# Optimization experiments

Hardware: AMD Instinct MI355X
Metric: run time of the kernel (lower is better)

The kernel has to match this reference:

```python
import jax, jax.numpy as jnp
import numpy as np

LN_EPS = 1e-3   # keras LayerNormalization default epsilon
EPS = 1e-5      # module's self.eps
QB = 128.0      # 2**(bits-1) with bits=8


def ste_round(x):
    # straight-through round: forward = round(x), backward = identity
    return x + jax.lax.stop_gradient(jnp.round(x) - x)


def setup_inputs() -> dict:
    key = jax.random.key(0)
    k1, k2 = jax.random.split(key)
    x = jax.random.normal(k1, (4, 8192, 1024), dtype=jnp.float32)
    weight = jax.random.normal(k2, (1024, 1024), dtype=jnp.float32) * 0.02
    ln_gamma = jnp.ones((1024,), dtype=jnp.float32)
    ln_beta = jnp.zeros((1024,), dtype=jnp.float32)
    return {"x": x, "weight": weight, "ln_gamma": ln_gamma, "ln_beta": ln_beta}


def reference(x, weight, ln_gamma, ln_beta):
    # LayerNorm over last axis (keras defaults: eps=1e-3, learnable scale/center)
    mu = jnp.mean(x, axis=-1, keepdims=True)
    var = jnp.var(x, axis=-1, keepdims=True)
    xn = (x - mu) * jax.lax.rsqrt(var + LN_EPS) * ln_gamma + ln_beta

    # 1.58-bit weight ternarization with STE round
    beta = jnp.mean(jnp.abs(weight))                     # per-tensor scale
    w_q = jnp.clip(ste_round(weight / (beta + EPS)), -1.0, 1.0)

    # activation quantization (flg_before_linear=True branch)
    gamma = jnp.max(jnp.abs(xn))                         # per-tensor absmax
    xq = jnp.clip(xn * QB / gamma, -QB + EPS, QB - EPS)

    # quantized matmul + fused rescale
    y = jnp.einsum('bsd,du->bsu', xq, w_q)
    return y * (gamma * beta / QB)
```

## Files before the change

kernel.cpp:

```cpp
#include <hip/hip_runtime.h>
#include <stdint.h>


#define M_ROWS 32768
#define KDIM 1024
#define NDIM 1024

typedef int v4i  __attribute__((ext_vector_type(4)));
typedef int v16i __attribute__((ext_vector_type(16)));

__global__ __launch_bounds__(256) void absum_k(const float* __restrict__ w,
                                               float* __restrict__ partials) {
    int idx = blockIdx.x * 256 + threadIdx.x;
    float4 v = ((const float4*)w)[idx];
    float s = fabsf(v.x) + fabsf(v.y) + fabsf(v.z) + fabsf(v.w);
    #pragma unroll
    for (int o = 32; o; o >>= 1) s += __shfl_xor(s, o);
    __shared__ float p[4];
    if ((threadIdx.x & 63) == 0) p[threadIdx.x >> 6] = s;
    __syncthreads();
    if (threadIdx.x == 0) partials[blockIdx.x] = p[0] + p[1] + p[2] + p[3];
}

__global__ __launch_bounds__(256) void quant_k(const float* __restrict__ w,
                                               const float* __restrict__ partials,
                                               char* __restrict__ wqT,
                                               float* __restrict__ wsum) {
    int t = threadIdx.x;
    float s = partials[t] + partials[t + 256] + partials[t + 512] + partials[t + 768];
    #pragma unroll
    for (int o = 32; o; o >>= 1) s += __shfl_xor(s, o);
    __shared__ float ps[4];
    if ((t & 63) == 0) ps[t >> 6] = s;
    __syncthreads();
    float total = ps[0] + ps[1] + ps[2] + ps[3];
    if (blockIdx.x == 0 && t == 0) wsum[0] = total;
    float beta = total * (1.0f / 1048576.0f);
    float inv  = 1.0f / (beta + 1e-5f);

    __shared__ char sT[64 * 80];
    int k0 = (blockIdx.x >> 4) * 64, n0 = (blockIdx.x & 15) * 64;
    int n_l = t & 63;
    #pragma unroll
    for (int r = 0; r < 16; ++r) {
        int k_l = (t >> 6) * 16 + r;
        float q = rintf(w[(size_t)(k0 + k_l) * NDIM + n0 + n_l] * inv);
        q = fminf(1.0f, fmaxf(-1.0f, q));
        sT[n_l * 80 + k_l] = (char)(int)q;
    }
    __syncthreads();
    int nn = t >> 2, c = t & 3;
    v4i val = *(const v4i*)&sT[nn * 80 + c * 16];
    *(v4i*)&wqT[(size_t)(n0 + nn) * KDIM + k0 + c * 16] = val;
}

__global__ __launch_bounds__(256) void ln_gemm_k(const float* __restrict__ x,
                                                 const float* __restrict__ g,
                                                 const float* __restrict__ bln,
                                                 const char* __restrict__ wq,
                                                 const float* __restrict__ wsum,
                                                 float* __restrict__ out) {
    __shared__ char  sA[64 * 1024];
    __shared__ char  sB[64 * 128];
    __shared__ float sScl[64];

    int t = threadIdx.x;
    int w = t >> 6, lane = t & 63;
    int half = lane >> 5, l31 = lane & 31;
    int bm0 = blockIdx.x * 64;

    int bn_l  = t >> 1;
    int bhalf = t & 1;
    int br    = t >> 2;

    v4i buf[2];
    {
        const char* src = wq + ((size_t)bn_l << 10) + bhalf * 32;
        buf[0] = *(const v4i*)(src);
        buf[1] = *(const v4i*)(src + 16);
    }

    float4 g4[4], b4[4];
    #pragma unroll
    for (int j = 0; j < 4; ++j) {
        g4[j] = ((const float4*)g)[lane + 64 * j];
        b4[j] = ((const float4*)bln)[lane + 64 * j];
    }
    #pragma unroll 1
    for (int rr = 0; rr < 16; ++rr) {
        int row = w * 16 + rr;
        const float4* xr = (const float4*)(x + ((size_t)(bm0 + row) << 10));
        float4 v0 = xr[lane], v1 = xr[lane + 64], v2 = xr[lane + 128], v3 = xr[lane + 192];
        float s  = v0.x + v0.y + v0.z + v0.w + v1.x + v1.y + v1.z + v1.w
                 + v2.x + v2.y + v2.z + v2.w + v3.x + v3.y + v3.z + v3.w;
        float ss = v0.x*v0.x + v0.y*v0.y + v0.z*v0.z + v0.w*v0.w
                 + v1.x*v1.x + v1.y*v1.y + v1.z*v1.z + v1.w*v1.w
                 + v2.x*v2.x + v2.y*v2.y + v2.z*v2.z + v2.w*v2.w
                 + v3.x*v3.x + v3.y*v3.y + v3.z*v3.z + v3.w*v3.w;
        #pragma unroll
        for (int o = 32; o; o >>= 1) { s += __shfl_xor(s, o); ss += __shfl_xor(ss, o); }
        float mu  = s * (1.0f / 1024.0f);
        float var = ss * (1.0f / 1024.0f) - mu * mu;
        float rs  = rsqrtf(var + 1e-3f);
        float xn[16];
        float4 vv[4] = {v0, v1, v2, v3};
        float mx = 0.f;
        #pragma unroll
        for (int j = 0; j < 4; ++j) {
            xn[4*j+0] = (vv[j].x - mu) * rs * g4[j].x + b4[j].x;
            xn[4*j+1] = (vv[j].y - mu) * rs * g4[j].y + b4[j].y;
            xn[4*j+2] = (vv[j].z - mu) * rs * g4[j].z + b4[j].z;
            xn[4*j+3] = (vv[j].w - mu) * rs * g4[j].w + b4[j].w;
            #pragma unroll
            for (int e = 0; e < 4; ++e) mx = fmaxf(mx, fabsf(xn[4*j+e]));
        }
        #pragma unroll
        for (int o = 32; o; o >>= 1) mx = fmaxf(mx, __shfl_xor(mx, o));
        mx = fmaxf(mx, 1e-20f);
        float inv = 127.0f / mx;
        if (lane == 0) sScl[row] = mx * (1.0f / 127.0f);
        #pragma unroll
        for (int j = 0; j < 4; ++j) {
            char4 c4;
            c4.x = (char)(int)rintf(xn[4*j+0] * inv);
            c4.y = (char)(int)rintf(xn[4*j+1] * inv);
            c4.z = (char)(int)rintf(xn[4*j+2] * inv);
            c4.w = (char)(int)rintf(xn[4*j+3] * inv);
            int c    = (lane >> 2) + 16 * j;
            int slot = c ^ (row & 7);
            *(char4*)&sA[row * 1024 + slot * 16 + (lane & 3) * 4] = c4;
        }
    }

    {
        #pragma unroll
        for (int q = 0; q < 2; ++q) {
            int slot = (((bn_l & 1) * 4 + bhalf * 2 + q) ^ (br & 7));
            *(v4i*)&sB[br * 128 + slot * 16] = buf[q];
        }
        const char* src = wq + ((size_t)bn_l << 10) + 64 + bhalf * 32;
        buf[0] = *(const v4i*)(src);
        buf[1] = *(const v4i*)(src + 16);
    }
    __syncthreads();

    int wm = w & 1, wn = w >> 1;
    int mrow  = wm * 32 + l31;
    int aBase = mrow * 1024;
    int am7   = mrow & 7;
    int nl0 = wn * 64 + l31;
    int br0 = nl0 >> 1, br1 = (nl0 + 32) >> 1;
    int bs0 = (nl0 & 1) * 4;
    float beta = wsum[0] * (1.0f / 1048576.0f);

    v16i acc[2];
    #pragma unroll
    for (int r = 0; r < 16; ++r) { acc[0][r] = 0; acc[1][r] = 0; }

    for (int it = 0; it < 128; ++it) {
        int kt = it & 15;
        #pragma unroll
        for (int kk = 0; kk < 2; ++kk) {
            int cA = kt * 4 + kk * 2 + half;
            v4i a  = *(const v4i*)&sA[aBase + ((cA ^ am7) << 4)];
            int ct = kk * 2 + half;
            v4i b0 = *(const v4i*)&sB[br0 * 128 + (((bs0 + ct) ^ (br0 & 7)) << 4)];
            v4i b1 = *(const v4i*)&sB[br1 * 128 + (((bs0 + ct) ^ (br1 & 7)) << 4)];
            acc[0] = __builtin_amdgcn_mfma_i32_32x32x32_i8(a, b0, acc[0], 0, 0, 0);
            acc[1] = __builtin_amdgcn_mfma_i32_32x32x32_i8(a, b1, acc[1], 0, 0, 0);
        }
        __syncthreads();
        if (it < 127) {
            #pragma unroll
            for (int q = 0; q < 2; ++q) {
                int slot = (((bn_l & 1) * 4 + bhalf * 2 + q) ^ (br & 7));
                *(v4i*)&sB[br * 128 + slot * 16] = buf[q];
            }
        }
        if (it < 126) {
            int tl = it + 2;
            const char* src = wq + ((size_t)(((tl >> 4) << 7) + bn_l) << 10)
                                 + (tl & 15) * 64 + bhalf * 32;
            buf[0] = *(const v4i*)(src);
            buf[1] = *(const v4i*)(src + 16);
        }
        if (kt == 15) {
            int n0 = it >> 4;
            int colBase = n0 * 128 + wn * 64 + l31;
            #pragma unroll
            for (int r = 0; r < 16; ++r) {
                int rloc = wm * 32 + (r & 3) + 8 * (r >> 2) + 4 * half;
                float sc = sScl[rloc] * beta;
                size_t o = (size_t)(bm0 + rloc) * NDIM + colBase;
                out[o]      = (float)acc[0][r] * sc;
                out[o + 32] = (float)acc[1][r] * sc;
            }
            #pragma unroll
            for (int r = 0; r < 16; ++r) { acc[0][r] = 0; acc[1][r] = 0; }
        }
        __syncthreads();
    }
}

extern "C" void kernel_launch(void* const* d_in, const int* in_sizes, int n_in,
                              void* d_out, int out_size, void* d_ws, size_t ws_size,
                              hipStream_t stream) {
    const float* x        = (const float*)d_in[0];
    const float* weight   = (const float*)d_in[1];
    const float* ln_gamma = (const float*)d_in[2];
    const float* ln_beta  = (const float*)d_in[3];
    float* out = (float*)d_out;

    float* wsum     = (float*)d_ws;
    float* partials = (float*)((char*)d_ws + 4096);
    char*  wqT      = (char*)d_ws + (1u << 18);

    absum_k<<<1024, 256, 0, stream>>>(weight, partials);
    quant_k<<<256, 256, 0, stream>>>(weight, partials, wqT, wsum);
    ln_gemm_k<<<M_ROWS / 64, 256, 0, stream>>>(x, ln_gamma, ln_beta, wqT, wsum, out);
}
```

Baseline: 289.0 us.

## Pre-pack weights into MFMA fragment layout and read B directly from global

The weight quantizer now writes int8 weights in a layout that matches the MFMA B-operand fragments, so the GEMM loads B straight from global/L2 into registers. This removes the shared-memory B staging and the two barriers per k-step. The A tile in LDS is re-laid out per lane, and each wave now computes a 64x128 output tile with 8 accumulators. LayerNorm loads become contiguous per lane. The cost is more register pressure (launch bounds 2) and every block rereading the full weight matrix from global memory.

Result: no change. 283.9 us (-1.8%).

```diff
diff --git a/kernel.cpp b/kernel.cpp
--- a/kernel.cpp
+++ b/kernel.cpp
@@ -24,7 +24,7 @@
 
 __global__ __launch_bounds__(256) void quant_k(const float* __restrict__ w,
                                                const float* __restrict__ partials,
-                                               char* __restrict__ wqT,
+                                               char* __restrict__ wqP,
                                                float* __restrict__ wsum) {
     int t = threadIdx.x;
     float s = partials[t] + partials[t + 256] + partials[t + 512] + partials[t + 768];
@@ -51,17 +51,18 @@
     __syncthreads();
     int nn = t >> 2, c = t & 3;
     v4i val = *(const v4i*)&sT[nn * 80 + c * 16];
-    *(v4i*)&wqT[(size_t)(n0 + nn) * KDIM + k0 + c * 16] = val;
-}
-
-__global__ __launch_bounds__(256) void ln_gemm_k(const float* __restrict__ x,
-                                                 const float* __restrict__ g,
-                                                 const float* __restrict__ bln,
-                                                 const char* __restrict__ wq,
-                                                 const float* __restrict__ wsum,
-                                                 float* __restrict__ out) {
+    int n = n0 + nn, k = k0 + c * 16;
+    int idx = ((n >> 5) * 32 + (k >> 5)) * 64 + (n & 31) + ((k >> 4) & 1) * 32;
+    *(v4i*)&wqP[(size_t)idx * 16] = val;
+}
+
+__global__ __launch_bounds__(256, 2) void ln_gemm_k(const float* __restrict__ x,
+                                                    const float* __restrict__ g,
+                                                    const float* __restrict__ bln,
+                                                    const char* __restrict__ wqP,
+                                                    const float* __restrict__ wsum,
+                                                    float* __restrict__ out) {
     __shared__ char  sA[64 * 1024];
-    __shared__ char  sB[64 * 128];
     __shared__ float sScl[64];
 
     int t = threadIdx.x;
@@ -69,28 +70,17 @@
     int half = lane >> 5, l31 = lane & 31;
     int bm0 = blockIdx.x * 64;
 
-    int bn_l  = t >> 1;
-    int bhalf = t & 1;
-    int br    = t >> 2;
-
-    v4i buf[2];
-    {
-        const char* src = wq + ((size_t)bn_l << 10) + bhalf * 32;
-        buf[0] = *(const v4i*)(src);
-        buf[1] = *(const v4i*)(src + 16);
-    }
-
     float4 g4[4], b4[4];
     #pragma unroll
     for (int j = 0; j < 4; ++j) {
-        g4[j] = ((const float4*)g)[lane + 64 * j];
-        b4[j] = ((const float4*)bln)[lane + 64 * j];
+        g4[j] = ((const float4*)g)[lane * 4 + j];
+        b4[j] = ((const float4*)bln)[lane * 4 + j];
     }
     #pragma unroll 1
     for (int rr = 0; rr < 16; ++rr) {
         int row = w * 16 + rr;
         const float4* xr = (const float4*)(x + ((size_t)(bm0 + row) << 10));
-        float4 v0 = xr[lane], v1 = xr[lane + 64], v2 = xr[lane + 128], v3 = xr[lane + 192];
+        float4 v0 = xr[lane * 4], v1 = xr[lane * 4 + 1], v2 = xr[lane * 4 + 2], v3 = xr[lane * 4 + 3];
         float s  = v0.x + v0.y + v0.z + v0.w + v1.x + v1.y + v1.z + v1.w
                  + v2.x + v2.y + v2.z + v2.w + v3.x + v3.y + v3.z + v3.w;
         float ss = v0.x*v0.x + v0.y*v0.y + v0.z*v0.z + v0.w*v0.w
@@ -119,86 +109,75 @@
         mx = fmaxf(mx, 1e-20f);
         float inv = 127.0f / mx;
         if (lane == 0) sScl[row] = mx * (1.0f / 127.0f);
+        int qw[4];
         #pragma unroll
         for (int j = 0; j < 4; ++j) {
-            char4 c4;
-            c4.x = (char)(int)rintf(xn[4*j+0] * inv);
-            c4.y = (char)(int)rintf(xn[4*j+1] * inv);
-            c4.z = (char)(int)rintf(xn[4*j+2] * inv);
-            c4.w = (char)(int)rintf(xn[4*j+3] * inv);
-            int c    = (lane >> 2) + 16 * j;
-            int slot = c ^ (row & 7);
-            *(char4*)&sA[row * 1024 + slot * 16 + (lane & 3) * 4] = c4;
-        }
-    }
-
-    {
-        #pragma unroll
-        for (int q = 0; q < 2; ++q) {
-            int slot = (((bn_l & 1) * 4 + bhalf * 2 + q) ^ (br & 7));
-            *(v4i*)&sB[br * 128 + slot * 16] = buf[q];
-        }
-        const char* src = wq + ((size_t)bn_l << 10) + 64 + bhalf * 32;
-        buf[0] = *(const v4i*)(src);
-        buf[1] = *(const v4i*)(src + 16);
-    }
-    __syncthreads();
-
-    int wm = w & 1, wn = w >> 1;
-    int mrow  = wm * 32 + l31;
-    int aBase = mrow * 1024;
-    int am7   = mrow & 7;
-    int nl0 = wn * 64 + l31;
-    int br0 = nl0 >> 1, br1 = (nl0 + 32) >> 1;
-    int bs0 = (nl0 & 1) * 4;
+            int b0 = (int)rintf(xn[4*j+0] * inv) & 255;
+            int b1 = (int)rintf(xn[4*j+1] * inv) & 255;
+            int b2 = (int)rintf(xn[4*j+2] * inv) & 255;
+            int b3 = (int)rintf(xn[4*j+3] * inv) & 255;
+            qw[j] = b0 | (b1 << 8) | (b2 << 16) | (b3 << 24);
+        }
+        v4i qv; qv[0] = qw[0]; qv[1] = qw[1]; qv[2] = qw[2]; qv[3] = qw[3];
+        int mf = row >> 5, r31 = row & 31;
+        int slot = r31 ^ (lane & 7);
+        *(v4i*)&sA[(((mf * 64 + lane) * 32) + slot) * 16] = qv;
+    }
+    __syncthreads();
+
     float beta = wsum[0] * (1.0f / 1048576.0f);
-
-    v16i acc[2];
-    #pragma unroll
-    for (int r = 0; r < 16; ++r) { acc[0][r] = 0; acc[1][r] = 0; }
-
-    for (int it = 0; it < 128; ++it) {
-        int kt = it & 15;
-        #pragma unroll
-        for (int kk = 0; kk < 2; ++kk) {
-            int cA = kt * 4 + kk * 2 + half;
-            v4i a  = *(const v4i*)&sA[aBase + ((cA ^ am7) << 4)];
-            int ct = kk * 2 + half;
-            v4i b0 = *(const v4i*)&sB[br0 * 128 + (((bs0 + ct) ^ (br0 & 7)) << 4)];
-            v4i b1 = *(const v4i*)&sB[br1 * 128 + (((bs0 + ct) ^ (br1 & 7)) << 4)];
-            acc[0] = __builtin_amdgcn_mfma_i32_32x32x32_i8(a, b0, acc[0], 0, 0, 0);
-            acc[1] = __builtin_amdgcn_mfma_i32_32x32x32_i8(a, b1, acc[1], 0, 0, 0);
-        }
-        __syncthreads();
-        if (it < 127) {
-            #pragma unroll
-            for (int q = 0; q < 2; ++q) {
-                int slot = (((bn_l & 1) * 4 + bhalf * 2 + q) ^ (br & 7));
-                *(v4i*)&sB[br * 128 + slot * 16] = buf[q];
+    const v4i* wp = (const v4i*)wqP;
+
+    #pragma unroll 1
+    for (int p = 0; p < 2; ++p) {
+        int nbB = p * 16 + w * 4;
+        v16i acc[2][4] = {};
+        v4i a0[2], a1[2], b0[4], b1[4];
+
+        #define LA(dst, S) do { \
+            int u_ = 2 * (S) + half; \
+            int o_ = ((u_ * 32) + (l31 ^ (u_ & 7))) * 16; \
+            dst[0] = *(const v4i*)&sA[o_]; \
+            dst[1] = *(const v4i*)&sA[o_ + 32768]; \
+        } while (0)
+        #define LB(dst, S) do { \
+            _Pragma("unroll") \
+            for (int j_ = 0; j_ < 4; ++j_) \
+                dst[j_] = wp[(size_t)(((nbB + j_) * 32 + (S)) * 64) + lane]; \
+        } while (0)
+
+        LB(b0, 0); LB(b1, 1); LA(a0, 0); LA(a1, 1);
+        #pragma unroll 1
+        for (int s = 0; s < 32; s += 2) {
+            #pragma unroll
+            for (int mf = 0; mf < 2; ++mf)
+                #pragma unroll
+                for (int j = 0; j < 4; ++j)
+                    acc[mf][j] = __builtin_amdgcn_mfma_i32_32x32x32_i8(a0[mf], b0[j], acc[mf][j], 0, 0, 0);
+            if (s + 2 < 32) { LB(b0, s + 2); LA(a0, s + 2); }
+            #pragma unroll
+            for (int mf = 0; mf < 2; ++mf)
+                #pragma unroll
+                for (int j = 0; j < 4; ++j)
+                    acc[mf][j] = __builtin_amdgcn_mfma_i32_32x32x32_i8(a1[mf], b1[j], acc[mf][j], 0, 0, 0);
+            if (s + 3 < 32) { LB(b1, s + 3); LA(a1, s + 3); }
+        }
+        #undef LA
+        #undef LB
+
+        #pragma unroll
+        for (int mf = 0; mf < 2; ++mf) {
+            #pragma unroll
+            for (int r = 0; r < 16; ++r) {
+                int rloc = mf * 32 + (r & 3) + 8 * (r >> 2) + 4 * half;
+                float sc = sScl[rloc] * beta;
+                size_t o = (size_t)(bm0 + rloc) * NDIM + p * 512 + w * 128 + l31;
+                out[o]      = (float)acc[0 + mf][0][r] * sc;
+                out[o + 32] = (float)acc[0 + mf][1][r] * sc;
+                out[o + 64] = (float)acc[0 + mf][2][r] * sc;
+                out[o + 96] = (float)acc[0 + mf][3][r] * sc;
             }
         }
-        if (it < 126) {
-            int tl = it + 2;
-            const char* src = wq + ((size_t)(((tl >> 4) << 7) + bn_l) << 10)
-                                 + (tl & 15) * 64 + bhalf * 32;
-            buf[0] = *(const v4i*)(src);
-            buf[1] = *(const v4i*)(src + 16);
-        }
-        if (kt == 15) {
-            int n0 = it >> 4;
-            int colBase = n0 * 128 + wn * 64 + l31;
-            #pragma unroll
-            for (int r = 0; r < 16; ++r) {
-                int rloc = wm * 32 + (r & 3) + 8 * (r >> 2) + 4 * half;
-                float sc = sScl[rloc] * beta;
-                size_t o = (size_t)(bm0 + rloc) * NDIM + colBase;
-                out[o]      = (float)acc[0][r] * sc;
-                out[o + 32] = (float)acc[1][r] * sc;
-            }
-            #pragma unroll
-            for (int r = 0; r < 16; ++r) { acc[0][r] = 0; acc[1][r] = 0; }
-        }
-        __syncthreads();
     }
 }
 
@@ -213,9 +192,9 @@
 
     float* wsum     = (float*)d_ws;
     float* partials = (float*)((char*)d_ws + 4096);
-    char*  wqT      = (char*)d_ws + (1u << 18);
+    char*  wqP      = (char*)d_ws + (1u << 18);
 
     absum_k<<<1024, 256, 0, stream>>>(weight, partials);
-    quant_k<<<256, 256, 0, stream>>>(weight, partials, wqT, wsum);
-    ln_gemm_k<<<M_ROWS / 64, 256, 0, stream>>>(x, ln_gamma, ln_beta, wqT, wsum, out);
-}
+    quant_k<<<256, 256, 0, stream>>>(weight, partials, wqP, wsum);
+    ln_gemm_k<<<M_ROWS / 64, 256, 0, stream>>>(x, ln_gamma, ln_beta, wqP, wsum, out);
+}
```
